# Kernel optimization log

Hardware: AMD Instinct MI355X
Metric: run time of the kernel (lower is better)

The kernel has to match this reference:

```python
import jax, jax.numpy as jnp
import numpy as np

B = 4096
FEAT = 40960
HID = 1024
L1 = 64
L2 = 32
P_ACTIVE = 30.0 / FEAT  # ~30 active features per position


def setup_inputs() -> dict:
    key = jax.random.key(0)
    ks = jax.random.split(key, 12)
    # Sparse binary HalfKP-style features
    white_features = (jax.random.uniform(ks[0], (B, FEAT)) < P_ACTIVE).astype(jnp.float32)
    black_features = (jax.random.uniform(ks[1], (B, FEAT)) < P_ACTIVE).astype(jnp.float32)
    stm = (jax.random.uniform(ks[2], (B, 1)) < 0.5).astype(jnp.float32)
    s = 0.02
    params = {
        'ft_w': jax.random.normal(ks[3], (HID, FEAT), jnp.float32) * s,
        'ft_b': jax.random.normal(ks[4], (HID,), jnp.float32) * s,
        'l1_w': jax.random.normal(ks[5], (L1, 2 * HID), jnp.float32) * s,
        'l1_b': jax.random.normal(ks[6], (L1,), jnp.float32) * s,
        'l2_w': jax.random.normal(ks[7], (L2, L1), jnp.float32) * s,
        'l2_b': jax.random.normal(ks[8], (L2,), jnp.float32) * s,
        'l3_w': jax.random.normal(ks[9], (1, L2), jnp.float32) * s,
        'l3_b': jax.random.normal(ks[10], (1,), jnp.float32) * s,
    }
    return dict(white_features=white_features, black_features=black_features, stm=stm, **params)


def reference(white_features, black_features, stm,
              ft_w, ft_b, l1_w, l1_b, l2_w, l2_b, l3_w, l3_b):
    # Feature transformer (shared weights, both perspectives)
    w = white_features @ ft_w.T + ft_b  # [B, HID]
    b = black_features @ ft_w.T + ft_b  # [B, HID]
    wb = jnp.concatenate([w, b], axis=1)  # [B, 2*HID]
    bw = jnp.concatenate([b, w], axis=1)
    acc = stm * wb + (1.0 - stm) * bw
    h1 = jnp.clip(acc, 0.0, 1.0)
    h2 = jnp.clip(h1 @ l1_w.T + l1_b, 0.0, 1.0)
    h3 = jnp.clip(h2 @ l2_w.T + l2_b, 0.0, 1.0)
    raw = h3 @ l3_w.T + l3_b  # [B, 1]
    return jax.nn.sigmoid(raw), raw
```

## Files before the change

kernel.cpp:

```cpp
#include <hip/hip_runtime.h>
#include <hip/hip_bf16.h>

#define B_SZ 4096
#define FEAT 40960
#define HID  1024
#define L1N  64
#define L2N  32
#define IDX_CAP 128
#define ROWS 4

static __device__ __forceinline__ unsigned short f2bf(float x) {
    __hip_bfloat16 h = __float2bfloat16(x);
    return *reinterpret_cast<unsigned short*>(&h);
}
static __device__ __forceinline__ float bf2f(unsigned short u) {
    unsigned int v = ((unsigned int)u) << 16;
    return __uint_as_float(v);
}
static __device__ __forceinline__ float clipf(float x) {
    return fminf(fmaxf(x, 0.0f), 1.0f);
}

__global__ __launch_bounds__(256) void transpose_ftw(
    const float* __restrict__ ftw, unsigned short* __restrict__ ftwT) {
    __shared__ float tile[32][65];
    const int tx = threadIdx.x;
    const int ty = threadIdx.y;
    const int f0 = blockIdx.x * 32;
    const int h0 = blockIdx.y * 64;
#pragma unroll
    for (int i = 0; i < 8; ++i) {
        int h = ty + 8 * i;
        tile[tx][h] = ftw[(size_t)(h0 + h) * FEAT + f0 + tx];
    }
    __syncthreads();
#pragma unroll
    for (int i = 0; i < 4; ++i) {
        int f = ty + 8 * i;
        float a = tile[f][2 * tx];
        float b = tile[f][2 * tx + 1];
        unsigned int pk = (unsigned int)f2bf(a) | ((unsigned int)f2bf(b) << 16);
        ((unsigned int*)(ftwT + (size_t)(f0 + f) * HID + h0))[tx] = pk;
    }
}

__global__ __launch_bounds__(256) void nnue_fused(
    const float* __restrict__ wf, const float* __restrict__ bfeat,
    const float* __restrict__ stm, const unsigned short* __restrict__ ftwT,
    const float* __restrict__ ftb,
    const float* __restrict__ l1w, const float* __restrict__ l1b,
    const float* __restrict__ l2w, const float* __restrict__ l2b,
    const float* __restrict__ l3w, const float* __restrict__ l3b,
    float* __restrict__ out) {

    __shared__ int  idx[2][ROWS][IDX_CAP];
    __shared__ int  cnt[2][ROWS];
    __shared__ float h1s[ROWS][2 * HID];
    __shared__ float4 part[4 * L1N];
    __shared__ float h2s[ROWS][L1N];
    __shared__ float h3s[ROWS][L2N];

    const int t = threadIdx.x;
    const int r0 = blockIdx.x * ROWS;

    if (t < 2 * ROWS) ((int*)cnt)[t] = 0;
    __syncthreads();

    for (int r = 0; r < ROWS; ++r) {
        const float4* wf4 = (const float4*)(wf + (size_t)(r0 + r) * FEAT);
        const float4* bf4 = (const float4*)(bfeat + (size_t)(r0 + r) * FEAT);
        for (int it = 0; it < (FEAT / 4) / 256; ++it) {
            int i4 = it * 256 + t;
            float4 wv = wf4[i4];
            float4 bv = bf4[i4];
            int base = i4 * 4;
            if (wv.x != 0.f) { int p = atomicAdd(&cnt[0][r], 1); if (p < IDX_CAP) idx[0][r][p] = base + 0; }
            if (wv.y != 0.f) { int p = atomicAdd(&cnt[0][r], 1); if (p < IDX_CAP) idx[0][r][p] = base + 1; }
            if (wv.z != 0.f) { int p = atomicAdd(&cnt[0][r], 1); if (p < IDX_CAP) idx[0][r][p] = base + 2; }
            if (wv.w != 0.f) { int p = atomicAdd(&cnt[0][r], 1); if (p < IDX_CAP) idx[0][r][p] = base + 3; }
            if (bv.x != 0.f) { int p = atomicAdd(&cnt[1][r], 1); if (p < IDX_CAP) idx[1][r][p] = base + 0; }
            if (bv.y != 0.f) { int p = atomicAdd(&cnt[1][r], 1); if (p < IDX_CAP) idx[1][r][p] = base + 1; }
            if (bv.z != 0.f) { int p = atomicAdd(&cnt[1][r], 1); if (p < IDX_CAP) idx[1][r][p] = base + 2; }
            if (bv.w != 0.f) { int p = atomicAdd(&cnt[1][r], 1); if (p < IDX_CAP) idx[1][r][p] = base + 3; }
        }
    }
    __syncthreads();

    float4 bias = ((const float4*)ftb)[t];
    float aw[ROWS][4], ab[ROWS][4];
#pragma unroll
    for (int r = 0; r < ROWS; ++r) {
        aw[r][0] = bias.x; aw[r][1] = bias.y; aw[r][2] = bias.z; aw[r][3] = bias.w;
        ab[r][0] = bias.x; ab[r][1] = bias.y; ab[r][2] = bias.z; ab[r][3] = bias.w;
    }
#pragma unroll
    for (int pp = 0; pp < 2; ++pp) {
        for (int r = 0; r < ROWS; ++r) {
            const int n = min(cnt[pp][r], IDX_CAP);
            float* acc = pp ? ab[r] : aw[r];
#pragma unroll 4
            for (int i = 0; i < n; ++i) {
                int f = idx[pp][r][i];
                ushort4 u = ((const ushort4*)(ftwT + (size_t)f * HID))[t];
                acc[0] += bf2f(u.x); acc[1] += bf2f(u.y);
                acc[2] += bf2f(u.z); acc[3] += bf2f(u.w);
            }
        }
    }

#pragma unroll
    for (int r = 0; r < ROWS; ++r) {
        const bool wfirst = (stm[r0 + r] != 0.0f);
#pragma unroll
        for (int c = 0; c < 4; ++c) {
            float fst = wfirst ? aw[r][c] : ab[r][c];
            float snd = wfirst ? ab[r][c] : aw[r][c];
            h1s[r][4 * t + c]       = clipf(fst);
            h1s[r][HID + 4 * t + c] = clipf(snd);
        }
    }
    __syncthreads();

    {
        const int k = t & 63, p = t >> 6;
        float a0 = 0.f, a1 = 0.f, a2 = 0.f, a3 = 0.f;
        const float4* w4 = (const float4*)(l1w + (size_t)k * 2 * HID + (size_t)p * 512);
        const int jbase = p * 512;
        for (int jj = 0; jj < 128; ++jj) {
            float4 w = w4[jj];
            int j = jbase + jj * 4;
            a0 += w.x * h1s[0][j] + w.y * h1s[0][j + 1] + w.z * h1s[0][j + 2] + w.w * h1s[0][j + 3];
            a1 += w.x * h1s[1][j] + w.y * h1s[1][j + 1] + w.z * h1s[1][j + 2] + w.w * h1s[1][j + 3];
            a2 += w.x * h1s[2][j] + w.y * h1s[2][j + 1] + w.z * h1s[2][j + 2] + w.w * h1s[2][j + 3];
            a3 += w.x * h1s[3][j] + w.y * h1s[3][j + 1] + w.z * h1s[3][j + 2] + w.w * h1s[3][j + 3];
        }
        part[p * L1N + k] = make_float4(a0, a1, a2, a3);
    }
    __syncthreads();
    if (t < L1N) {
        float4 s0 = part[t], s1 = part[L1N + t], s2 = part[2 * L1N + t], s3 = part[3 * L1N + t];
        float b1 = l1b[t];
        h2s[0][t] = clipf(s0.x + s1.x + s2.x + s3.x + b1);
        h2s[1][t] = clipf(s0.y + s1.y + s2.y + s3.y + b1);
        h2s[2][t] = clipf(s0.z + s1.z + s2.z + s3.z + b1);
        h2s[3][t] = clipf(s0.w + s1.w + s2.w + s3.w + b1);
    }
    __syncthreads();

    if (t < ROWS * L2N) {
        int r = t >> 5, k2 = t & 31;
        float a = l2b[k2];
        for (int j = 0; j < L1N; ++j) a += h2s[r][j] * l2w[k2 * L1N + j];
        h3s[r][k2] = clipf(a);
    }
    __syncthreads();

    if (t < ROWS) {
        float raw = l3b[0];
        for (int j = 0; j < L2N; ++j) raw += h3s[t][j] * l3w[j];
        out[r0 + t] = 1.0f / (1.0f + expf(-raw));
        out[B_SZ + r0 + t] = raw;
    }
}

extern "C" void kernel_launch(void* const* d_in, const int* in_sizes, int n_in,
                              void* d_out, int out_size, void* d_ws, size_t ws_size,
                              hipStream_t stream) {
    const float* wf    = (const float*)d_in[0];
    const float* bfeat = (const float*)d_in[1];
    const float* stm   = (const float*)d_in[2];
    const float* ftw   = (const float*)d_in[3];
    const float* ftb   = (const float*)d_in[4];
    const float* l1w   = (const float*)d_in[5];
    const float* l1b   = (const float*)d_in[6];
    const float* l2w   = (const float*)d_in[7];
    const float* l2b   = (const float*)d_in[8];
    const float* l3w   = (const float*)d_in[9];
    const float* l3b   = (const float*)d_in[10];
    float* out = (float*)d_out;

    unsigned short* ftwT = (unsigned short*)d_ws;

    transpose_ftw<<<dim3(FEAT / 32, HID / 64), dim3(32, 8), 0, stream>>>(ftw, ftwT);
    nnue_fused<<<B_SZ / ROWS, 256, 0, stream>>>(wf, bfeat, stm, ftwT, ftb,
                                                l1w, l1b, l2w, l2b, l3w, l3b, out);
}
```

Before: 1.515 ms.

## Split sparse feature scan into its own wide kernel, pack h1 as bf16

Moves the dense scan of the white and black feature matrices out of the fused kernel into a separate kernel with one block per row and perspective. That gives 8192 blocks streaming the inputs instead of 1024 blocks each doing sequential per-row loops. Active indices and counts go through a workspace, and the gather/MLP kernel loads them from there. The h1 activations are also stored in shared memory as packed bf16, which halves LDS use and may improve occupancy but costs some precision in layer 1.

```diff
diff --git a/kernel.cpp b/kernel.cpp
--- a/kernel.cpp
+++ b/kernel.cpp
@@ -17,6 +17,15 @@
     unsigned int v = ((unsigned int)u) << 16;
     return __uint_as_float(v);
 }
+static __device__ __forceinline__ float bf2f_lo(unsigned int u) {
+    return __uint_as_float(u << 16);
+}
+static __device__ __forceinline__ float bf2f_hi(unsigned int u) {
+    return __uint_as_float(u & 0xffff0000u);
+}
+static __device__ __forceinline__ unsigned int packbf(float lo, float hi) {
+    return (unsigned int)f2bf(lo) | ((unsigned int)f2bf(hi) << 16);
+}
 static __device__ __forceinline__ float clipf(float x) {
     return fminf(fmaxf(x, 0.0f), 1.0f);
 }
@@ -37,25 +46,51 @@
 #pragma unroll
     for (int i = 0; i < 4; ++i) {
         int f = ty + 8 * i;
-        float a = tile[f][2 * tx];
-        float b = tile[f][2 * tx + 1];
-        unsigned int pk = (unsigned int)f2bf(a) | ((unsigned int)f2bf(b) << 16);
+        unsigned int pk = packbf(tile[f][2 * tx], tile[f][2 * tx + 1]);
         ((unsigned int*)(ftwT + (size_t)(f0 + f) * HID + h0))[tx] = pk;
     }
 }
 
-__global__ __launch_bounds__(256) void nnue_fused(
+__global__ __launch_bounds__(256) void scan_kernel(
     const float* __restrict__ wf, const float* __restrict__ bfeat,
+    int* __restrict__ idx_ws, int* __restrict__ cnt_ws) {
+    __shared__ int cnt;
+    const int t = threadIdx.x;
+    const int b = blockIdx.x;
+    const int persp = b >> 12;
+    const int row   = b & (B_SZ - 1);
+    const float4* s4 = (const float4*)((persp ? bfeat : wf) + (size_t)row * FEAT);
+    int* dst = idx_ws + (size_t)b * IDX_CAP;
+
+    if (t == 0) cnt = 0;
+    __syncthreads();
+
+#pragma unroll 4
+    for (int it = 0; it < (FEAT / 4) / 256; ++it) {
+        int i4 = it * 256 + t;
+        float4 v = s4[i4];
+        int base = i4 * 4;
+        if (v.x != 0.f) { int p = atomicAdd(&cnt, 1); if (p < IDX_CAP) dst[p] = base + 0; }
+        if (v.y != 0.f) { int p = atomicAdd(&cnt, 1); if (p < IDX_CAP) dst[p] = base + 1; }
+        if (v.z != 0.f) { int p = atomicAdd(&cnt, 1); if (p < IDX_CAP) dst[p] = base + 2; }
+        if (v.w != 0.f) { int p = atomicAdd(&cnt, 1); if (p < IDX_CAP) dst[p] = base + 3; }
+    }
+    __syncthreads();
+    if (t == 0) cnt_ws[b] = min(cnt, IDX_CAP);
+}
+
+__global__ __launch_bounds__(256) void gather_mlp(
     const float* __restrict__ stm, const unsigned short* __restrict__ ftwT,
     const float* __restrict__ ftb,
+    const int* __restrict__ idx_ws, const int* __restrict__ cnt_ws,
     const float* __restrict__ l1w, const float* __restrict__ l1b,
     const float* __restrict__ l2w, const float* __restrict__ l2b,
     const float* __restrict__ l3w, const float* __restrict__ l3b,
     float* __restrict__ out) {
 
-    __shared__ int  idx[2][ROWS][IDX_CAP];
-    __shared__ int  cnt[2][ROWS];
-    __shared__ float h1s[ROWS][2 * HID];
+    __shared__ int idxs[2 * ROWS][IDX_CAP];
+    __shared__ int cnts[2 * ROWS];
+    __shared__ unsigned int h1p[ROWS][HID];
     __shared__ float4 part[4 * L1N];
     __shared__ float h2s[ROWS][L1N];
     __shared__ float h3s[ROWS][L2N];
@@ -63,61 +98,56 @@
     const int t = threadIdx.x;
     const int r0 = blockIdx.x * ROWS;
 
-    if (t < 2 * ROWS) ((int*)cnt)[t] = 0;
-    __syncthreads();
-
-    for (int r = 0; r < ROWS; ++r) {
-        const float4* wf4 = (const float4*)(wf + (size_t)(r0 + r) * FEAT);
-        const float4* bf4 = (const float4*)(bfeat + (size_t)(r0 + r) * FEAT);
-        for (int it = 0; it < (FEAT / 4) / 256; ++it) {
-            int i4 = it * 256 + t;
-            float4 wv = wf4[i4];
-            float4 bv = bf4[i4];
-            int base = i4 * 4;
-            if (wv.x != 0.f) { int p = atomicAdd(&cnt[0][r], 1); if (p < IDX_CAP) idx[0][r][p] = base + 0; }
-            if (wv.y != 0.f) { int p = atomicAdd(&cnt[0][r], 1); if (p < IDX_CAP) idx[0][r][p] = base + 1; }
-            if (wv.z != 0.f) { int p = atomicAdd(&cnt[0][r], 1); if (p < IDX_CAP) idx[0][r][p] = base + 2; }
-            if (wv.w != 0.f) { int p = atomicAdd(&cnt[0][r], 1); if (p < IDX_CAP) idx[0][r][p] = base + 3; }
-            if (bv.x != 0.f) { int p = atomicAdd(&cnt[1][r], 1); if (p < IDX_CAP) idx[1][r][p] = base + 0; }
-            if (bv.y != 0.f) { int p = atomicAdd(&cnt[1][r], 1); if (p < IDX_CAP) idx[1][r][p] = base + 1; }
-            if (bv.z != 0.f) { int p = atomicAdd(&cnt[1][r], 1); if (p < IDX_CAP) idx[1][r][p] = base + 2; }
-            if (bv.w != 0.f) { int p = atomicAdd(&cnt[1][r], 1); if (p < IDX_CAP) idx[1][r][p] = base + 3; }
+    if (t < 2 * ROWS) {
+        int pp = t >> 2, r = t & 3;
+        cnts[t] = cnt_ws[pp * B_SZ + r0 + r];
+    }
+    for (int i = t; i < 2 * ROWS * IDX_CAP; i += 256) {
+        int l = i >> 7;
+        int pp = l >> 2, r = l & 3;
+        idxs[l][i & (IDX_CAP - 1)] =
+            idx_ws[(size_t)(pp * B_SZ + r0 + r) * IDX_CAP + (i & (IDX_CAP - 1))];
+    }
+    __syncthreads();
+
+    float4 bias = ((const float4*)ftb)[t];
+    float acc[2][ROWS][4];
+#pragma unroll
+    for (int pp = 0; pp < 2; ++pp)
+#pragma unroll
+        for (int r = 0; r < ROWS; ++r) {
+            acc[pp][r][0] = bias.x; acc[pp][r][1] = bias.y;
+            acc[pp][r][2] = bias.z; acc[pp][r][3] = bias.w;
         }
-    }
-    __syncthreads();
-
-    float4 bias = ((const float4*)ftb)[t];
-    float aw[ROWS][4], ab[ROWS][4];
-#pragma unroll
-    for (int r = 0; r < ROWS; ++r) {
-        aw[r][0] = bias.x; aw[r][1] = bias.y; aw[r][2] = bias.z; aw[r][3] = bias.w;
-        ab[r][0] = bias.x; ab[r][1] = bias.y; ab[r][2] = bias.z; ab[r][3] = bias.w;
-    }
-#pragma unroll
-    for (int pp = 0; pp < 2; ++pp) {
+
+#pragma unroll
+    for (int pp = 0; pp < 2; ++pp)
+#pragma unroll
         for (int r = 0; r < ROWS; ++r) {
-            const int n = min(cnt[pp][r], IDX_CAP);
-            float* acc = pp ? ab[r] : aw[r];
+            const int n = cnts[pp * ROWS + r];
+            float* a = acc[pp][r];
 #pragma unroll 4
             for (int i = 0; i < n; ++i) {
-                int f = idx[pp][r][i];
+                int f = idxs[pp * ROWS + r][i];
                 ushort4 u = ((const ushort4*)(ftwT + (size_t)f * HID))[t];
-                acc[0] += bf2f(u.x); acc[1] += bf2f(u.y);
-                acc[2] += bf2f(u.z); acc[3] += bf2f(u.w);
+                a[0] += bf2f(u.x); a[1] += bf2f(u.y);
+                a[2] += bf2f(u.z); a[3] += bf2f(u.w);
             }
         }
-    }
 
 #pragma unroll
     for (int r = 0; r < ROWS; ++r) {
         const bool wfirst = (stm[r0 + r] != 0.0f);
-#pragma unroll
-        for (int c = 0; c < 4; ++c) {
-            float fst = wfirst ? aw[r][c] : ab[r][c];
-            float snd = wfirst ? ab[r][c] : aw[r][c];
-            h1s[r][4 * t + c]       = clipf(fst);
-            h1s[r][HID + 4 * t + c] = clipf(snd);
-        }
+        const float* fw = acc[0][r];
+        const float* fb = acc[1][r];
+        float f0 = wfirst ? fw[0] : fb[0], f1 = wfirst ? fw[1] : fb[1];
+        float f2 = wfirst ? fw[2] : fb[2], f3 = wfirst ? fw[3] : fb[3];
+        float s0 = wfirst ? fb[0] : fw[0], s1 = wfirst ? fb[1] : fw[1];
+        float s2 = wfirst ? fb[2] : fw[2], s3 = wfirst ? fb[3] : fw[3];
+        h1p[r][2 * t]           = packbf(clipf(f0), clipf(f1));
+        h1p[r][2 * t + 1]       = packbf(clipf(f2), clipf(f3));
+        h1p[r][512 + 2 * t]     = packbf(clipf(s0), clipf(s1));
+        h1p[r][512 + 2 * t + 1] = packbf(clipf(s2), clipf(s3));
     }
     __syncthreads();
 
@@ -125,14 +155,18 @@
         const int k = t & 63, p = t >> 6;
         float a0 = 0.f, a1 = 0.f, a2 = 0.f, a3 = 0.f;
         const float4* w4 = (const float4*)(l1w + (size_t)k * 2 * HID + (size_t)p * 512);
-        const int jbase = p * 512;
+        const int qbase = p * 256;
         for (int jj = 0; jj < 128; ++jj) {
             float4 w = w4[jj];
-            int j = jbase + jj * 4;
-            a0 += w.x * h1s[0][j] + w.y * h1s[0][j + 1] + w.z * h1s[0][j + 2] + w.w * h1s[0][j + 3];
-            a1 += w.x * h1s[1][j] + w.y * h1s[1][j + 1] + w.z * h1s[1][j + 2] + w.w * h1s[1][j + 3];
-            a2 += w.x * h1s[2][j] + w.y * h1s[2][j + 1] + w.z * h1s[2][j + 2] + w.w * h1s[2][j + 3];
-            a3 += w.x * h1s[3][j] + w.y * h1s[3][j + 1] + w.z * h1s[3][j + 2] + w.w * h1s[3][j + 3];
+            int q = qbase + 2 * jj;
+            unsigned int u00 = h1p[0][q], u01 = h1p[0][q + 1];
+            unsigned int u10 = h1p[1][q], u11 = h1p[1][q + 1];
+            unsigned int u20 = h1p[2][q], u21 = h1p[2][q + 1];
+            unsigned int u30 = h1p[3][q], u31 = h1p[3][q + 1];
+            a0 += w.x * bf2f_lo(u00) + w.y * bf2f_hi(u00) + w.z * bf2f_lo(u01) + w.w * bf2f_hi(u01);
+            a1 += w.x * bf2f_lo(u10) + w.y * bf2f_hi(u10) + w.z * bf2f_lo(u11) + w.w * bf2f_hi(u11);
+            a2 += w.x * bf2f_lo(u20) + w.y * bf2f_hi(u20) + w.z * bf2f_lo(u21) + w.w * bf2f_hi(u21);
+            a3 += w.x * bf2f_lo(u30) + w.y * bf2f_hi(u30) + w.z * bf2f_lo(u31) + w.w * bf2f_hi(u31);
         }
         part[p * L1N + k] = make_float4(a0, a1, a2, a3);
     }
@@ -180,8 +214,11 @@
     float* out = (float*)d_out;
 
     unsigned short* ftwT = (unsigned short*)d_ws;
+    int* idx_ws = (int*)(ftwT + (size_t)FEAT * HID);
+    int* cnt_ws = idx_ws + (size_t)2 * B_SZ * IDX_CAP;
 
     transpose_ftw<<<dim3(FEAT / 32, HID / 64), dim3(32, 8), 0, stream>>>(ftw, ftwT);
-    nnue_fused<<<B_SZ / ROWS, 256, 0, stream>>>(wf, bfeat, stm, ftwT, ftb,
+    scan_kernel<<<2 * B_SZ, 256, 0, stream>>>(wf, bfeat, idx_ws, cnt_ws);
+    gather_mlp<<<B_SZ / ROWS, 256, 0, stream>>>(stm, ftwT, ftb, idx_ws, cnt_ws,
                                                 l1w, l1b, l2w, l2b, l3w, l3b, out);
 }
```

Measured after the change: 1.459 ms. 3.7% less time.
